# Kernel tuning notes

Hardware: AMD Instinct MI355X
Metric: run time of the kernel (lower is better)

The kernel has to match this reference:

```python
import jax, jax.numpy as jnp
import numpy as np

IN_FEATURES = 2048
OUT_FEATURES = 2048
LOG_DIM = 11                      # ceil(log2(2048))
BUTTERFLY_DIM = 2 ** LOG_DIM      # 2048
MAX_BLOCKS = BUTTERFLY_DIM // 2   # 1024 (layer 0 has the most blocks)
BATCH = 16384


def setup_inputs() -> dict:
    key = jax.random.key(0)
    ks = jax.random.split(key, 5)
    x = jax.random.normal(ks[0], (BATCH, IN_FEATURES), dtype=jnp.float32)
    # Linear weights stored torch-style: [out, in]
    w_in = jax.random.normal(ks[1], (BUTTERFLY_DIM, IN_FEATURES), dtype=jnp.float32) * 0.02
    w_out = jax.random.normal(ks[2], (OUT_FEATURES, BUTTERFLY_DIM), dtype=jnp.float32) * 0.02
    b_out = jnp.zeros((OUT_FEATURES,), dtype=jnp.float32)
    # Per-stage rotation params: theta = rand*0.01, a=cos(theta), b=sin(theta).
    # Stage l uses num_blocks = BUTTERFLY_DIM // 2^(l+1) entries; pad to MAX_BLOCKS.
    theta = jax.random.uniform(ks[3], (LOG_DIM, MAX_BLOCKS), dtype=jnp.float32) * 0.01
    a_pad = jnp.cos(theta)
    b_pad = jnp.sin(theta)
    return {"x": x, "w_in": w_in, "w_out": w_out, "b_out": b_out,
            "a_pad": a_pad, "b_pad": b_pad}


def _butterfly(x, a_pad, b_pad):
    # x: [B, BUTTERFLY_DIM]
    B = x.shape[0]
    for l in range(LOG_DIM):
        block_size = 2 ** l
        num_blocks = BUTTERFLY_DIM // (2 * block_size)
        a = a_pad[l, :num_blocks][None, :, None]  # [1, nb, 1]
        b = b_pad[l, :num_blocks][None, :, None]
        xv = x.reshape(B, num_blocks, 2, block_size)
        x0 = xv[:, :, 0, :]
        x1 = xv[:, :, 1, :]
        top = a * x0 + b * x1
        bot = -b * x0 + a * x1
        x = jnp.stack([top, bot], axis=2).reshape(B, BUTTERFLY_DIM)
    return x


def reference(x, w_in, w_out, b_out, a_pad, b_pad):
    h = x @ w_in.T                      # [B, BUTTERFLY_DIM]
    h = _butterfly(h, a_pad, b_pad)
    return h @ w_out.T + b_out          # [B, OUT_FEATURES]
```

## Files before the change

kernel.cpp:

```cpp
#include <hip/hip_runtime.h>
#include <hip/hip_bf16.h>

using bf16 = __hip_bfloat16;
using bf16x8 = __attribute__((ext_vector_type(8))) __bf16;
using f32x4 = __attribute__((ext_vector_type(4))) float;

typedef const __attribute__((address_space(1))) void* gas_ptr;
typedef __attribute__((address_space(3))) void* las_ptr;
#define LOAD_LDS16(g, l) \
    __builtin_amdgcn_global_load_lds((gas_ptr)(const void*)(g), (las_ptr)(void*)(l), 16, 0, 0)

#define LOG_DIM 11
#define BDIM 2048
#define NFEAT 2048
#define BATCH 16384

__device__ __forceinline__ void cvt_chunk(const float* __restrict__ x,
                                          bf16* __restrict__ x_bf, int chunk, int tid) {
    #pragma unroll
    for (int it = 0; it < 16; ++it) {
        size_t i = ((size_t)chunk * 16 + it) * 2048 + tid * 8;
        float4 v0 = *(const float4*)(x + i);
        float4 v1 = *(const float4*)(x + i + 4);
        union { bf16 h[8]; int4 v; } u;
        u.h[0] = __float2bfloat16(v0.x); u.h[1] = __float2bfloat16(v0.y);
        u.h[2] = __float2bfloat16(v0.z); u.h[3] = __float2bfloat16(v0.w);
        u.h[4] = __float2bfloat16(v1.x); u.h[5] = __float2bfloat16(v1.y);
        u.h[6] = __float2bfloat16(v1.z); u.h[7] = __float2bfloat16(v1.w);
        *(int4*)(x_bf + i) = u.v;
    }
}

__global__ __launch_bounds__(256) void prep1(const float* __restrict__ w_out,
                                             const float* __restrict__ a_pad,
                                             const float* __restrict__ b_pad,
                                             const float* __restrict__ w_in,
                                             bf16* __restrict__ woutb,
                                             bf16* __restrict__ wint,
                                             const float* __restrict__ x,
                                             bf16* __restrict__ x_bf) {
    __shared__ float v[BDIM];
    __shared__ float tile[32][33];
    const int t = threadIdx.x;
    if (blockIdx.x < 1024) {
        cvt_chunk(x, x_bf, blockIdx.x, t);
    } else if (blockIdx.x < 3072) {
        const int o = blockIdx.x - 1024;
        const float* row = w_out + (size_t)o * BDIM;
        for (int i = t; i < BDIM / 4; i += 256)
            ((float4*)v)[i] = ((const float4*)row)[i];
        __syncthreads();
        for (int l = LOG_DIM - 1; l >= 0; --l) {
            #pragma unroll
            for (int pp = 0; pp < 4; ++pp) {
                int p = t + pp * 256;
                int j = p >> l;
                int s = p & ((1 << l) - 1);
                int i0 = (j << (l + 1)) | s;
                int i1 = i0 + (1 << l);
                float a = a_pad[l * (BDIM / 2) + j];
                float b = b_pad[l * (BDIM / 2) + j];
                float x0 = v[i0], x1 = v[i1];
                v[i0] = a * x0 - b * x1;
                v[i1] = b * x0 + a * x1;
            }
            __syncthreads();
        }
        union { bf16 h[8]; int4 vv; } u;
        #pragma unroll
        for (int j = 0; j < 8; ++j) u.h[j] = __float2bfloat16(v[t * 8 + j]);
        *(int4*)(woutb + (size_t)o * BDIM + t * 8) = u.vv;
    } else {
        const int b = blockIdx.x - 3072;
        const int bx = b & 63, by = b >> 6;
        const int tx = t & 31, ty = t >> 5;
        #pragma unroll
        for (int r = ty; r < 32; r += 8)
            tile[r][tx] = w_in[(size_t)(by * 32 + r) * NFEAT + bx * 32 + tx];
        __syncthreads();
        #pragma unroll
        for (int r = ty; r < 32; r += 8)
            wint[(size_t)(bx * 32 + r) * NFEAT + by * 32 + tx] = __float2bfloat16(tile[tx][r]);
    }
}

#define GK 2048
#define LDS_SLOT 65536
#define LDS_BOFF 32768
#define LDS_KH 16384

__global__ __launch_bounds__(512, 2) void gemmM_sk(const bf16* __restrict__ A,
                                                   const bf16* __restrict__ Bt,
                                                   bf16* __restrict__ part) {
    __shared__ __align__(16) char lds[131072];

    const int tid = threadIdx.x;
    const int wave = tid >> 6, lane = tid & 63;
    const int l15 = lane & 15, kc = lane >> 4;
    const int wm = wave >> 2, wn = wave & 3;

    const int mBase = blockIdx.y * 256, nBase = blockIdx.x * 256;
    const int kz = blockIdx.z;
    bf16* C = part + (size_t)kz * GK * GK;

    const int c_log = tid ^ ((tid >> 3) & 3);
    const int srow = c_log >> 2, skc = c_log & 3;
    const bf16* gA = A + (size_t)(mBase + srow) * GK + kz * 512 + skc * 8;
    const bf16* gB = Bt + (size_t)(nBase + srow) * GK + kz * 512 + skc * 8;
    const int stgBase = wave * 1024;

    const int kcx = kc ^ ((l15 >> 1) & 3);
    const int aoff = wm * 8192 + l15 * 64 + kcx * 16;
    const int boff = LDS_BOFF + wn * 4096 + l15 * 64 + kcx * 16;

    f32x4 acc[8][4];
    #pragma unroll
    for (int i = 0; i < 8; ++i)
        #pragma unroll
        for (int j = 0; j < 4; ++j) acc[i][j] = (f32x4){0.f, 0.f, 0.f, 0.f};

    bf16x8 Af[4], Bf[4];

#define STG(GSRC, LDSC, KT, KH) do {                                        \
    const bf16* _g = (GSRC) + (KT) * 64 + (KH) * 32;                        \
    LOAD_LDS16(_g, lds + (LDSC) + stgBase);                                 \
    LOAD_LDS16(_g + (size_t)128 * GK, lds + (LDSC) + stgBase + 8192);       \
} while (0)

#define READP(SLOT, KH, MH, DOB) do {                                       \
    const int _rb = (SLOT) * LDS_SLOT + (KH) * LDS_KH;                      \
    _Pragma("unroll")                                                       \
    for (int _f = 0; _f < 4; ++_f)                                          \
        Af[_f] = *(const bf16x8*)(lds + _rb + aoff + (MH) * 4096 + _f * 1024); \
    if (DOB) {                                                              \
        _Pragma("unroll")                                                   \
        for (int _f = 0; _f < 4; ++_f)                                      \
            Bf[_f] = *(const bf16x8*)(lds + _rb + boff + _f * 1024);        \
    }                                                                       \
} while (0)

    STG(gA, 0 * LDS_SLOT + 0, 0, 0);
    STG(gB, 0 * LDS_SLOT + LDS_BOFF + 0, 0, 0);
    STG(gA, 0 * LDS_SLOT + LDS_KH, 0, 1);
    STG(gB, 0 * LDS_SLOT + LDS_BOFF + LDS_KH, 0, 1);
    STG(gA, 1 * LDS_SLOT + 0, 1, 0);
    STG(gB, 1 * LDS_SLOT + LDS_BOFF + 0, 1, 0);
    STG(gB, 1 * LDS_SLOT + LDS_BOFF + LDS_KH, 1, 1);
    asm volatile("s_waitcnt vmcnt(6)");
    __builtin_amdgcn_s_barrier();

#define PH(S, KH, MH, DOB, SGSRC, SLDS, SKT, SKH, DOVM) do {                \
    READP(S, KH, MH, DOB);                                                  \
    STG(SGSRC, SLDS, SKT, SKH);                                             \
    if (DOVM) asm volatile("s_waitcnt vmcnt(6)");                           \
    __builtin_amdgcn_sched_barrier(0);                                      \
    __builtin_amdgcn_s_barrier();                                           \
    asm volatile("s_waitcnt lgkmcnt(0)");                                   \
    __builtin_amdgcn_sched_barrier(0);                                      \
    __builtin_amdgcn_s_setprio(1);                                          \
    _Pragma("unroll")                                                       \
    for (int _mf = 0; _mf < 4; ++_mf)                                       \
        _Pragma("unroll")                                                   \
        for (int _nf = 0; _nf < 4; ++_nf)                                   \
            acc[(MH) * 4 + _mf][_nf] = __builtin_amdgcn_mfma_f32_16x16x32_bf16( \
                Af[_mf], Bf[_nf], acc[(MH) * 4 + _mf][_nf], 0, 0, 0);       \
    __builtin_amdgcn_s_setprio(0);                                          \
    __builtin_amdgcn_s_barrier();                                           \
} while (0)

    for (int it = 0; it < 4; ++it) {
        const int t0 = 2 * it;
        const int t1 = (t0 + 1) & 7, t2 = (t0 + 2) & 7, t3 = (t0 + 3) & 7;
        PH(0, 0, 0, 1, gA, 1 * LDS_SLOT + LDS_KH,            t1, 1, 0);
        PH(0, 0, 1, 0, gB, 0 * LDS_SLOT + LDS_BOFF,          t2, 0, 0);
        PH(0, 1, 0, 1, gA, 0 * LDS_SLOT + 0,                 t2, 0, 0);
        PH(0, 1, 1, 0, gB, 0 * LDS_SLOT + LDS_BOFF + LDS_KH, t2, 1, 1);
        PH(1, 0, 0, 1, gA, 0 * LDS_SLOT + LDS_KH,            t2, 1, 0);
        PH(1, 0, 1, 0, gB, 1 * LDS_SLOT + LDS_BOFF,          t3, 0, 0);
        PH(1, 1, 0, 1, gA, 1 * LDS_SLOT + 0,                 t3, 0, 0);
        PH(1, 1, 1, 0, gB, 1 * LDS_SLOT + LDS_BOFF + LDS_KH, t3, 1, 1);
    }

    const int cRow0 = mBase + wm * 128 + (lane >> 4) * 4;
    const int cCol0 = nBase + wn * 64 + l15;
    #pragma unroll
    for (int Mf = 0; Mf < 8; ++Mf)
        #pragma unroll
        for (int nf = 0; nf < 4; ++nf)
            #pragma unroll
            for (int r = 0; r < 4; ++r)
                C[(size_t)(cRow0 + Mf * 16 + r) * GK + cCol0 + nf * 16] =
                    __float2bfloat16(acc[Mf][nf][r]);
#undef PH
#undef READP
#undef STG
}

__global__ __launch_bounds__(256) void addcvt4(const bf16* __restrict__ p,
                                               bf16* __restrict__ out) {
    size_t i = ((size_t)blockIdx.x * 256 + threadIdx.x) * 8;
    constexpr size_t STRIDE = (size_t)2048 * 2048;
    float s[8];
    #pragma unroll
    for (int j = 0; j < 8; ++j) s[j] = 0.f;
    #pragma unroll
    for (int z = 0; z < 4; ++z) {
        union { bf16 h[8]; int4 v; } a;
        a.v = *(const int4*)(p + z * STRIDE + i);
        #pragma unroll
        for (int j = 0; j < 8; ++j) s[j] += __bfloat162float(a.h[j]);
    }
    union { bf16 h[8]; int4 v; } o;
    #pragma unroll
    for (int j = 0; j < 8; ++j) o.h[j] = __float2bfloat16(s[j]);
    *(int4*)(out + i) = o.v;
}

__global__ __launch_bounds__(512, 2) void gemm256(const bf16* __restrict__ A,
                                                  const bf16* __restrict__ Bt,
                                                  const float* __restrict__ bias,
                                                  float* __restrict__ C) {
    __shared__ __align__(16) char lds[131072];

    const int tid = threadIdx.x;
    const int wave = tid >> 6, lane = tid & 63;
    const int l15 = lane & 15, kc = lane >> 4;
    const int wm = wave >> 2, wn = wave & 3;

    const int bid = blockIdx.x;
    const int swz = (bid & 7) * 64 + (bid >> 3);
    const int bm = swz >> 3, bn = swz & 7;
    const int mBase = bm * 256, nBase = bn * 256;

    const int c_log = tid ^ ((tid >> 3) & 3);
    const int srow = c_log >> 2, skc = c_log & 3;
    const bf16* gA = A + (size_t)(mBase + srow) * GK + skc * 8;
    const bf16* gB = Bt + (size_t)(nBase + srow) * GK + skc * 8;
    const int stgBase = wave * 1024;

    const int kcx = kc ^ ((l15 >> 1) & 3);
    const int aoff = wm * 8192 + l15 * 64 + kcx * 16;
    const int boff = LDS_BOFF + wn * 4096 + l15 * 64 + kcx * 16;

    f32x4 acc[8][4];
    #pragma unroll
    for (int i = 0; i < 8; ++i)
        #pragma unroll
        for (int j = 0; j < 4; ++j) acc[i][j] = (f32x4){0.f, 0.f, 0.f, 0.f};

    bf16x8 Af[4], Bf[4];

#define STG(GSRC, LDSC, KT, KH) do {                                        \
    const bf16* _g = (GSRC) + (KT) * 64 + (KH) * 32;                        \
    LOAD_LDS16(_g, lds + (LDSC) + stgBase);                                 \
    LOAD_LDS16(_g + (size_t)128 * GK, lds + (LDSC) + stgBase + 8192);       \
} while (0)

#define READP(SLOT, KH, MH, DOB) do {                                       \
    const int _rb = (SLOT) * LDS_SLOT + (KH) * LDS_KH;                      \
    _Pragma("unroll")                                                       \
    for (int _f = 0; _f < 4; ++_f)                                          \
        Af[_f] = *(const bf16x8*)(lds + _rb + aoff + (MH) * 4096 + _f * 1024); \
    if (DOB) {                                                              \
        _Pragma("unroll")                                                   \
        for (int _f = 0; _f < 4; ++_f)                                      \
            Bf[_f] = *(const bf16x8*)(lds + _rb + boff + _f * 1024);        \
    }                                                                       \
} while (0)

    STG(gA, 0 * LDS_SLOT + 0, 0, 0);
    STG(gB, 0 * LDS_SLOT + LDS_BOFF + 0, 0, 0);
    STG(gA, 0 * LDS_SLOT + LDS_KH, 0, 1);
    STG(gB, 0 * LDS_SLOT + LDS_BOFF + LDS_KH, 0, 1);
    STG(gA, 1 * LDS_SLOT + 0, 1, 0);
    STG(gB, 1 * LDS_SLOT + LDS_BOFF + 0, 1, 0);
    STG(gB, 1 * LDS_SLOT + LDS_BOFF + LDS_KH, 1, 1);
    asm volatile("s_waitcnt vmcnt(6)");
    __builtin_amdgcn_s_barrier();

#define PH(S, KH, MH, DOB, SGSRC, SLDS, SKT, SKH, DOVM) do {                \
    READP(S, KH, MH, DOB);                                                  \
    STG(SGSRC, SLDS, SKT, SKH);                                             \
    if (DOVM) asm volatile("s_waitcnt vmcnt(6)");                           \
    __builtin_amdgcn_sched_barrier(0);                                      \
    __builtin_amdgcn_s_barrier();                                           \
    asm volatile("s_waitcnt lgkmcnt(0)");                                   \
    __builtin_amdgcn_sched_barrier(0);                                      \
    __builtin_amdgcn_s_setprio(1);                                          \
    _Pragma("unroll")                                                       \
    for (int _mf = 0; _mf < 4; ++_mf)                                       \
        _Pragma("unroll")                                                   \
        for (int _nf = 0; _nf < 4; ++_nf)                                   \
            acc[(MH) * 4 + _mf][_nf] = __builtin_amdgcn_mfma_f32_16x16x32_bf16( \
                Af[_mf], Bf[_nf], acc[(MH) * 4 + _mf][_nf], 0, 0, 0);       \
    __builtin_amdgcn_s_setprio(0);                                          \
    __builtin_amdgcn_s_barrier();                                           \
} while (0)

    for (int it = 0; it < 16; ++it) {
        const int t0 = 2 * it;
        const int t1 = (t0 + 1) & 31, t2 = (t0 + 2) & 31, t3 = (t0 + 3) & 31;
        PH(0, 0, 0, 1, gA, 1 * LDS_SLOT + LDS_KH,            t1, 1, 0);
        PH(0, 0, 1, 0, gB, 0 * LDS_SLOT + LDS_BOFF,          t2, 0, 0);
        PH(0, 1, 0, 1, gA, 0 * LDS_SLOT + 0,                 t2, 0, 0);
        PH(0, 1, 1, 0, gB, 0 * LDS_SLOT + LDS_BOFF + LDS_KH, t2, 1, 1);
        PH(1, 0, 0, 1, gA, 0 * LDS_SLOT + LDS_KH,            t2, 1, 0);
        PH(1, 0, 1, 0, gB, 1 * LDS_SLOT + LDS_BOFF,          t3, 0, 0);
        PH(1, 1, 0, 1, gA, 1 * LDS_SLOT + 0,                 t3, 0, 0);
        PH(1, 1, 1, 0, gB, 1 * LDS_SLOT + LDS_BOFF + LDS_KH, t3, 1, 1);
    }

    const int cRow0 = mBase + wm * 128 + (lane >> 4) * 4;
    const int cCol0 = nBase + wn * 64 + l15;
    float bv[4];
    #pragma unroll
    for (int nf = 0; nf < 4; ++nf) bv[nf] = bias[cCol0 + nf * 16];
    #pragma unroll
    for (int Mf = 0; Mf < 8; ++Mf)
        #pragma unroll
        for (int nf = 0; nf < 4; ++nf)
            #pragma unroll
            for (int r = 0; r < 4; ++r)
                C[(size_t)(cRow0 + Mf * 16 + r) * GK + cCol0 + nf * 16] =
                    acc[Mf][nf][r] + bv[nf];
#undef PH
#undef READP
#undef STG
}

extern "C" void kernel_launch(void* const* d_in, const int* in_sizes, int n_in,
                              void* d_out, int out_size, void* d_ws, size_t ws_size,
                              hipStream_t stream) {
    const float* x     = (const float*)d_in[0];
    const float* w_in  = (const float*)d_in[1];
    const float* w_out = (const float*)d_in[2];
    const float* b_out = (const float*)d_in[3];
    const float* a_pad = (const float*)d_in[4];
    const float* b_pad = (const float*)d_in[5];
    float* out = (float*)d_out;

    char* ws = (char*)d_ws;
    bf16* x_bf  = (bf16*)ws;
    bf16* woutb = (bf16*)(ws + (size_t)67108864);
    bf16* wint  = (bf16*)(ws + (size_t)75497472);
    bf16* mcomb = (bf16*)(ws + (size_t)83886080);

    bf16* part = (bf16*)d_out;

    prep1<<<dim3(7168), dim3(256), 0, stream>>>(w_out, a_pad, b_pad, w_in,
                                                woutb, wint, x, x_bf);
    gemmM_sk<<<dim3(8, 8, 4), dim3(512), 0, stream>>>(woutb, wint, part);
    addcvt4<<<dim3(NFEAT * BDIM / (256 * 8)), dim3(256), 0, stream>>>(part, mcomb);
    gemm256<<<dim3((BATCH / 256) * (NFEAT / 256)), dim3(512), 0, stream>>>(
        x_bf, mcomb, b_out, out);
}
```

Before: 226.0 us.

## Fuse fp32-to-bf16 conversion of x into the main GEMM A-operand load

Removes the separate pass that converted x to bf16 in the workspace. The main GEMM now loads fp32 x through registers, converts to bf16, and writes to LDS, with software-pipelined register double-buffering of the A tiles. This drops a 128MB read plus 64MB write round trip. In exchange the GEMM reads twice the bytes for A, uses more registers, and stages A through VGPRs instead of direct-to-LDS loads, all inside a reworked barrier schedule.

```diff
diff --git a/kernel.cpp b/kernel.cpp
--- a/kernel.cpp
+++ b/kernel.cpp
@@ -14,38 +14,18 @@
 #define BDIM 2048
 #define NFEAT 2048
 #define BATCH 16384
-
-__device__ __forceinline__ void cvt_chunk(const float* __restrict__ x,
-                                          bf16* __restrict__ x_bf, int chunk, int tid) {
-    #pragma unroll
-    for (int it = 0; it < 16; ++it) {
-        size_t i = ((size_t)chunk * 16 + it) * 2048 + tid * 8;
-        float4 v0 = *(const float4*)(x + i);
-        float4 v1 = *(const float4*)(x + i + 4);
-        union { bf16 h[8]; int4 v; } u;
-        u.h[0] = __float2bfloat16(v0.x); u.h[1] = __float2bfloat16(v0.y);
-        u.h[2] = __float2bfloat16(v0.z); u.h[3] = __float2bfloat16(v0.w);
-        u.h[4] = __float2bfloat16(v1.x); u.h[5] = __float2bfloat16(v1.y);
-        u.h[6] = __float2bfloat16(v1.z); u.h[7] = __float2bfloat16(v1.w);
-        *(int4*)(x_bf + i) = u.v;
-    }
-}
 
 __global__ __launch_bounds__(256) void prep1(const float* __restrict__ w_out,
                                              const float* __restrict__ a_pad,
                                              const float* __restrict__ b_pad,
                                              const float* __restrict__ w_in,
                                              bf16* __restrict__ woutb,
-                                             bf16* __restrict__ wint,
-                                             const float* __restrict__ x,
-                                             bf16* __restrict__ x_bf) {
+                                             bf16* __restrict__ wint) {
     __shared__ float v[BDIM];
     __shared__ float tile[32][33];
     const int t = threadIdx.x;
-    if (blockIdx.x < 1024) {
-        cvt_chunk(x, x_bf, blockIdx.x, t);
-    } else if (blockIdx.x < 3072) {
-        const int o = blockIdx.x - 1024;
+    if (blockIdx.x < 2048) {
+        const int o = blockIdx.x;
         const float* row = w_out + (size_t)o * BDIM;
         for (int i = t; i < BDIM / 4; i += 256)
             ((float4*)v)[i] = ((const float4*)row)[i];
@@ -71,7 +51,7 @@
         for (int j = 0; j < 8; ++j) u.h[j] = __float2bfloat16(v[t * 8 + j]);
         *(int4*)(woutb + (size_t)o * BDIM + t * 8) = u.vv;
     } else {
-        const int b = blockIdx.x - 3072;
+        const int b = blockIdx.x - 2048;
         const int bx = b & 63, by = b >> 6;
         const int tx = t & 31, ty = t >> 5;
         #pragma unroll
@@ -216,7 +196,7 @@
     *(int4*)(out + i) = o.v;
 }
 
-__global__ __launch_bounds__(512, 2) void gemm256(const bf16* __restrict__ A,
+__global__ __launch_bounds__(512, 2) void gemm256(const float* __restrict__ X,
                                                   const bf16* __restrict__ Bt,
                                                   const float* __restrict__ bias,
                                                   float* __restrict__ C) {
@@ -234,9 +214,10 @@
 
     const int c_log = tid ^ ((tid >> 3) & 3);
     const int srow = c_log >> 2, skc = c_log & 3;
-    const bf16* gA = A + (size_t)(mBase + srow) * GK + skc * 8;
+    const float* xA = X + (size_t)(mBase + srow) * GK + skc * 8;
     const bf16* gB = Bt + (size_t)(nBase + srow) * GK + skc * 8;
     const int stgBase = wave * 1024;
+    const int sOff = tid * 16;
 
     const int kcx = kc ^ ((l15 >> 1) & 3);
     const int aoff = wm * 8192 + l15 * 64 + kcx * 16;
@@ -249,11 +230,34 @@
         for (int j = 0; j < 4; ++j) acc[i][j] = (f32x4){0.f, 0.f, 0.f, 0.f};
 
     bf16x8 Af[4], Bf[4];
-
-#define STG(GSRC, LDSC, KT, KH) do {                                        \
-    const bf16* _g = (GSRC) + (KT) * 64 + (KH) * 32;                        \
+    float4 Ra0, Ra1, Ra2, Ra3, Rb0, Rb1, Rb2, Rb3;
+
+#define STGB(LDSC, KT, KH) do {                                             \
+    const bf16* _g = gB + (KT) * 64 + (KH) * 32;                            \
     LOAD_LDS16(_g, lds + (LDSC) + stgBase);                                 \
     LOAD_LDS16(_g + (size_t)128 * GK, lds + (LDSC) + stgBase + 8192);       \
+} while (0)
+
+#define AISSUE(R0, R1, R2, R3, KT, KH) do {                                 \
+    const float* _g = xA + (KT) * 64 + (KH) * 32;                           \
+    R0 = *(const float4*)(_g);                                              \
+    R1 = *(const float4*)(_g + 4);                                          \
+    R2 = *(const float4*)(_g + (size_t)128 * GK);                           \
+    R3 = *(const float4*)(_g + (size_t)128 * GK + 4);                       \
+} while (0)
+
+#define AWRITE(R0, R1, R2, R3, WLDSC) do {                                  \
+    union { bf16 h[8]; int4 v; } _u0, _u1;                                  \
+    _u0.h[0] = __float2bfloat16(R0.x); _u0.h[1] = __float2bfloat16(R0.y);   \
+    _u0.h[2] = __float2bfloat16(R0.z); _u0.h[3] = __float2bfloat16(R0.w);   \
+    _u0.h[4] = __float2bfloat16(R1.x); _u0.h[5] = __float2bfloat16(R1.y);   \
+    _u0.h[6] = __float2bfloat16(R1.z); _u0.h[7] = __float2bfloat16(R1.w);   \
+    _u1.h[0] = __float2bfloat16(R2.x); _u1.h[1] = __float2bfloat16(R2.y);   \
+    _u1.h[2] = __float2bfloat16(R2.z); _u1.h[3] = __float2bfloat16(R2.w);   \
+    _u1.h[4] = __float2bfloat16(R3.x); _u1.h[5] = __float2bfloat16(R3.y);   \
+    _u1.h[6] = __float2bfloat16(R3.z); _u1.h[7] = __float2bfloat16(R3.w);   \
+    *(int4*)(lds + (WLDSC) + sOff) = _u0.v;                                 \
+    *(int4*)(lds + (WLDSC) + sOff + 8192) = _u1.v;                          \
 } while (0)
 
 #define READP(SLOT, KH, MH, DOB) do {                                       \
@@ -268,24 +272,7 @@
     }                                                                       \
 } while (0)
 
-    STG(gA, 0 * LDS_SLOT + 0, 0, 0);
-    STG(gB, 0 * LDS_SLOT + LDS_BOFF + 0, 0, 0);
-    STG(gA, 0 * LDS_SLOT + LDS_KH, 0, 1);
-    STG(gB, 0 * LDS_SLOT + LDS_BOFF + LDS_KH, 0, 1);
-    STG(gA, 1 * LDS_SLOT + 0, 1, 0);
-    STG(gB, 1 * LDS_SLOT + LDS_BOFF + 0, 1, 0);
-    STG(gB, 1 * LDS_SLOT + LDS_BOFF + LDS_KH, 1, 1);
-    asm volatile("s_waitcnt vmcnt(6)");
-    __builtin_amdgcn_s_barrier();
-
-#define PH(S, KH, MH, DOB, SGSRC, SLDS, SKT, SKH, DOVM) do {                \
-    READP(S, KH, MH, DOB);                                                  \
-    STG(SGSRC, SLDS, SKT, SKH);                                             \
-    if (DOVM) asm volatile("s_waitcnt vmcnt(6)");                           \
-    __builtin_amdgcn_sched_barrier(0);                                      \
-    __builtin_amdgcn_s_barrier();                                           \
-    asm volatile("s_waitcnt lgkmcnt(0)");                                   \
-    __builtin_amdgcn_sched_barrier(0);                                      \
+#define MFMAS(MH)                                                           \
     __builtin_amdgcn_s_setprio(1);                                          \
     _Pragma("unroll")                                                       \
     for (int _mf = 0; _mf < 4; ++_mf)                                       \
@@ -293,21 +280,64 @@
         for (int _nf = 0; _nf < 4; ++_nf)                                   \
             acc[(MH) * 4 + _mf][_nf] = __builtin_amdgcn_mfma_f32_16x16x32_bf16( \
                 Af[_mf], Bf[_nf], acc[(MH) * 4 + _mf][_nf], 0, 0, 0);       \
-    __builtin_amdgcn_s_setprio(0);                                          \
-    __builtin_amdgcn_s_barrier();                                           \
-} while (0)
+    __builtin_amdgcn_s_setprio(0);
+
+#define APH(S, KH, MH, W0, W1, W2, W3, WLDSC, I0, I1, I2, I3, IKT, IKH) do {\
+    AISSUE(I0, I1, I2, I3, IKT, IKH);                                       \
+    __builtin_amdgcn_sched_barrier(0);                                      \
+    asm volatile("s_waitcnt vmcnt(6)");                                     \
+    AWRITE(W0, W1, W2, W3, WLDSC);                                          \
+    READP(S, KH, MH, 1);                                                    \
+    __builtin_amdgcn_sched_barrier(0);                                      \
+    __builtin_amdgcn_s_barrier();                                           \
+    asm volatile("s_waitcnt lgkmcnt(0)");                                   \
+    __builtin_amdgcn_sched_barrier(0);                                      \
+    MFMAS(MH)                                                               \
+    __builtin_amdgcn_s_barrier();                                           \
+} while (0)
+
+#define BPH(S, KH, MH, BLDSC, BKT, BKH) do {                                \
+    READP(S, KH, MH, 0);                                                    \
+    STGB(BLDSC, BKT, BKH);                                                  \
+    __builtin_amdgcn_sched_barrier(0);                                      \
+    __builtin_amdgcn_s_barrier();                                           \
+    asm volatile("s_waitcnt lgkmcnt(0)");                                   \
+    __builtin_amdgcn_sched_barrier(0);                                      \
+    MFMAS(MH)                                                               \
+    __builtin_amdgcn_s_barrier();                                           \
+} while (0)
+
+    STGB(0 * LDS_SLOT + LDS_BOFF + 0, 0, 0);
+    STGB(0 * LDS_SLOT + LDS_BOFF + LDS_KH, 0, 1);
+    STGB(1 * LDS_SLOT + LDS_BOFF + 0, 1, 0);
+    STGB(1 * LDS_SLOT + LDS_BOFF + LDS_KH, 1, 1);
+    AISSUE(Ra0, Ra1, Ra2, Ra3, 0, 0);
+    AWRITE(Ra0, Ra1, Ra2, Ra3, 0 * LDS_SLOT + 0);
+    AISSUE(Ra0, Ra1, Ra2, Ra3, 0, 1);
+    AWRITE(Ra0, Ra1, Ra2, Ra3, 0 * LDS_SLOT + LDS_KH);
+    AISSUE(Ra0, Ra1, Ra2, Ra3, 1, 0);
+    AWRITE(Ra0, Ra1, Ra2, Ra3, 1 * LDS_SLOT + 0);
+    AISSUE(Ra0, Ra1, Ra2, Ra3, 1, 1);
+    asm volatile("s_waitcnt lgkmcnt(0)");
+    __builtin_amdgcn_sched_barrier(0);
+    __builtin_amdgcn_s_barrier();
 
     for (int it = 0; it < 16; ++it) {
         const int t0 = 2 * it;
         const int t1 = (t0 + 1) & 31, t2 = (t0 + 2) & 31, t3 = (t0 + 3) & 31;
-        PH(0, 0, 0, 1, gA, 1 * LDS_SLOT + LDS_KH,            t1, 1, 0);
-        PH(0, 0, 1, 0, gB, 0 * LDS_SLOT + LDS_BOFF,          t2, 0, 0);
-        PH(0, 1, 0, 1, gA, 0 * LDS_SLOT + 0,                 t2, 0, 0);
-        PH(0, 1, 1, 0, gB, 0 * LDS_SLOT + LDS_BOFF + LDS_KH, t2, 1, 1);
-        PH(1, 0, 0, 1, gA, 0 * LDS_SLOT + LDS_KH,            t2, 1, 0);
-        PH(1, 0, 1, 0, gB, 1 * LDS_SLOT + LDS_BOFF,          t3, 0, 0);
-        PH(1, 1, 0, 1, gA, 1 * LDS_SLOT + 0,                 t3, 0, 0);
-        PH(1, 1, 1, 0, gB, 1 * LDS_SLOT + LDS_BOFF + LDS_KH, t3, 1, 1);
+        (void)t1;
+        APH(0, 0, 0, Ra0, Ra1, Ra2, Ra3, 1 * LDS_SLOT + LDS_KH,
+                     Rb0, Rb1, Rb2, Rb3, t2, 0);
+        BPH(0, 0, 1, 0 * LDS_SLOT + LDS_BOFF, t2, 0);
+        APH(0, 1, 0, Rb0, Rb1, Rb2, Rb3, 0 * LDS_SLOT + 0,
+                     Ra0, Ra1, Ra2, Ra3, t2, 1);
+        BPH(0, 1, 1, 0 * LDS_SLOT + LDS_BOFF + LDS_KH, t2, 1);
+        APH(1, 0, 0, Ra0, Ra1, Ra2, Ra3, 0 * LDS_SLOT + LDS_KH,
+                     Rb0, Rb1, Rb2, Rb3, t3, 0);
+        BPH(1, 0, 1, 1 * LDS_SLOT + LDS_BOFF, t3, 0);
+        APH(1, 1, 0, Rb0, Rb1, Rb2, Rb3, 1 * LDS_SLOT + 0,
+                     Ra0, Ra1, Ra2, Ra3, t3, 1);
+        BPH(1, 1, 1, 1 * LDS_SLOT + LDS_BOFF + LDS_KH, t3, 1);
     }
 
     const int cRow0 = mBase + wm * 128 + (lane >> 4) * 4;
@@ -323,9 +353,13 @@
             for (int r = 0; r < 4; ++r)
                 C[(size_t)(cRow0 + Mf * 16 + r) * GK + cCol0 + nf * 16] =
                     acc[Mf][nf][r] + bv[nf];
-#undef PH
+#undef APH
+#undef BPH
+#undef MFMAS
 #undef READP
-#undef STG
+#undef AWRITE
+#undef AISSUE
+#undef STGB
 }
 
 extern "C" void kernel_launch(void* const* d_in, const int* in_sizes, int n_in,
@@ -340,17 +374,16 @@
     float* out = (float*)d_out;
 
     char* ws = (char*)d_ws;
-    bf16* x_bf  = (bf16*)ws;
-    bf16* woutb = (bf16*)(ws + (size_t)67108864);
-    bf16* wint  = (bf16*)(ws + (size_t)75497472);
-    bf16* mcomb = (bf16*)(ws + (size_t)83886080);
+    bf16* woutb = (bf16*)ws;
+    bf16* wint  = (bf16*)(ws + (size_t)8388608);
+    bf16* mcomb = (bf16*)(ws + (size_t)16777216);
 
     bf16* part = (bf16*)d_out;
 
-    prep1<<<dim3(7168), dim3(256), 0, stream>>>(w_out, a_pad, b_pad, w_in,
-                                                woutb, wint, x, x_bf);
+    prep1<<<dim3(6144), dim3(256), 0, stream>>>(w_out, a_pad, b_pad, w_in,
+                                                woutb, wint);
     gemmM_sk<<<dim3(8, 8, 4), dim3(512), 0, stream>>>(woutb, wint, part);
     addcvt4<<<dim3(NFEAT * BDIM / (256 * 8)), dim3(256), 0, stream>>>(part, mcomb);
     gemm256<<<dim3((BATCH / 256) * (NFEAT / 256)), dim3(512), 0, stream>>>(
-        x_bf, mcomb, b_out, out);
-}
+        x, mcomb, b_out, out);
+}
```

New measurement: 274.8 us. 1.22x slower.
